# Kernel tuning notes

Hardware: AMD Instinct MI355X
Metric: run time of the kernel (lower is better)

## Reference

```python
import jax, jax.numpy as jnp
import numpy as np
import math

N, E = 50000, 800000
N_BASIS, N_ATOM, L = 32, 128, 2
START, STOP = 0.0, 10.0

_idx = [(i, j, L - i - j) for i in range(L + 1) for j in range(L + 1 - i)]
IP = np.array([t[0] for t in _idx], np.float32)
JP = np.array([t[1] for t in _idx], np.float32)
KP = np.array([t[2] for t in _idx], np.float32)
_d = np.array([math.factorial(a) * math.factorial(b) * math.factorial(c) for a, b, c in _idx], np.float32)
PREF2 = np.sqrt(math.factorial(L) / _d).astype(np.float32)  # [T], T = (L+1)(L+2)/2 = 6
OFFSETS = np.linspace(START, STOP, N_BASIS, dtype=np.float32)
WIDTH = np.float32(OFFSETS[1] - OFFSETS[0])


def _signed_pow(x, p):
    # matches torch.pow for negative base with integer-valued float exponent
    p = np.asarray(p)
    odd = (p.astype(np.int64) % 2 == 1)
    r = jnp.abs(x)[:, None] ** jnp.asarray(p)[None, :]
    return jnp.where((x < 0.0)[:, None] & jnp.asarray(odd)[None, :], -r, r)


def setup_inputs() -> dict:
    key = jax.random.key(0)
    ks = jax.random.split(key, 12)
    s = 0.05
    return {
        "feat": jax.random.normal(ks[0], (N, N_ATOM), jnp.float32),
        "dis_vec": jax.random.normal(ks[1], (E, 3), jnp.float32),
        "cj_w1": jax.random.normal(ks[2], (N_ATOM, N_ATOM), jnp.float32) * s,
        "cj_b1": jnp.zeros((N_ATOM,), jnp.float32),
        "cj_w2": jax.random.normal(ks[3], (N_ATOM, 1), jnp.float32) * s,
        "cj_b2": jnp.zeros((1,), jnp.float32),
        "msg_w1": jax.random.normal(ks[4], (N_BASIS, N_ATOM), jnp.float32) * s,
        "msg_b1": jnp.zeros((N_ATOM,), jnp.float32),
        "msg_w2": jax.random.normal(ks[5], (N_ATOM, N_ATOM), jnp.float32) * s,
        "msg_b2": jnp.zeros((N_ATOM,), jnp.float32),
        "filt_w1": jax.random.normal(ks[6], (IP.shape[0], IP.shape[0]), jnp.float32) * s,
        "filt_w2": jax.random.normal(ks[7], (IP.shape[0], 1), jnp.float32) * s,
        "filt_b2": jnp.zeros((1,), jnp.float32),
        "src": jax.random.randint(ks[8], (E,), 0, N, jnp.int32),
        "dst": jax.random.randint(ks[9], (E,), 0, N, jnp.int32),
    }


def reference(feat, dis_vec, cj_w1, cj_b1, cj_w2, cj_b2, msg_w1, msg_b1, msg_w2, msg_b2, filt_w1, filt_w2, filt_b2, src, dst):
    silu = jax.nn.silu  # swish
    # polynomial prefactor: [E, T]
    phix = _signed_pow(dis_vec[:, 0] + 1e-8, IP)
    phiy = _signed_pow(dis_vec[:, 1] + 1e-8, JP)
    phiz = _signed_pow(dis_vec[:, 2] + 1e-8, KP)
    prefactor = phix * phiy * phiz
    # gaussian basis: [E, n_basis] (cutoff_network is None -> C = 1)
    dis = jnp.linalg.norm(dis_vec + 1e-9, axis=-1)
    coeff = -0.5 / (WIDTH ** 2)
    g0 = jnp.exp(coeff * (dis[:, None] - jnp.asarray(OFFSETS)[None, :]) ** 2)
    # gauss: [E, n_basis, T]
    gauss = prefactor[:, None, :] * g0[:, :, None] * jnp.asarray(PREF2)[None, None, :]
    # cj = cj_mlp(feat): [N, 1]
    cj = silu(feat @ cj_w1 + cj_b1) @ cj_w2 + cj_b2
    # e_mul_v: gather dst-node scalar onto edges; copy_e_sum(g.reverse()): scatter-sum to src nodes
    fij = gauss * cj[dst][:, :, None]  # [E, n_basis, T]
    agg = jax.ops.segment_sum(fij, src, num_segments=N)  # [N, n_basis, T]
    f2 = jnp.sum(agg ** 2, axis=-1)  # [N, n_basis]
    msg_in = f2 / (jnp.linalg.norm(f2 + 1e-9, axis=-1, keepdims=True) + 1.0)
    msg_out = silu(msg_in @ msg_w1 + msg_b1) @ msg_w2 + msg_b2  # [N, n_atom_basis]
    gn = gauss / (jnp.linalg.norm(gauss + 1e-8, axis=-1) + 1.0)[..., None]
    filt = (silu(gn @ filt_w1) @ filt_w2 + filt_b2)[..., 0]  # [E, n_basis]
    return msg_out, filt
```

## Files before the change

kernel.cpp:

```cpp
#include <hip/hip_runtime.h>
#include <math.h>

#define N_NODES 50000
#define N_EDGES 800000
#define NB 32
#define NA 128

constexpr double STEP_D = 10.0 / 31.0;
constexpr float  STEP_F = (float)(10.0 / 31.0);
constexpr float  COEFF  = -0.5f / (STEP_F * STEP_F);
constexpr float  R2     = 1.41421356237309515f;
constexpr float  INV_STEP = 3.1f;
constexpr float  HWIN   = 2.05f;

__device__ __forceinline__ float fast_rcp(float x) {
    return __builtin_amdgcn_rcpf(x);
}

__device__ __forceinline__ float silu_f(float x) {
    return x * fast_rcp(1.0f + __expf(-x));
}

__global__ __launch_bounds__(256) void k_cj(const float* __restrict__ feat,
                                            const float* __restrict__ w1,
                                            const float* __restrict__ b1,
                                            const float* __restrict__ w2,
                                            const float* __restrict__ b2,
                                            float* __restrict__ cj) {
    __shared__ float fls[64 * 128];
    int tid = threadIdx.x;
    int jq  = tid & 31;
    int ng  = tid >> 5;
    int j0  = jq * 4;
    int n0  = blockIdx.x * 64;

    {
        const float4* fp = (const float4*)feat;
        int base = n0 * 32;
        int maxi = N_NODES * 32 - 1;
#pragma unroll
        for (int r = 0; r < 8; r++) {
            int idx = base + r * 256 + tid;
            ((float4*)fls)[r * 256 + tid] = fp[min(idx, maxi)];
        }
    }
    __syncthreads();

    float4 bv = *(const float4*)&b1[j0];
    float h[8][4];
#pragma unroll
    for (int i = 0; i < 8; i++) {
        h[i][0] = bv.x; h[i][1] = bv.y; h[i][2] = bv.z; h[i][3] = bv.w;
    }
    for (int kb = 0; kb < 128; kb += 4) {
        float4 wv[4];
#pragma unroll
        for (int u = 0; u < 4; u++) wv[u] = *(const float4*)&w1[(kb + u) * 128 + j0];
#pragma unroll
        for (int i = 0; i < 8; i++) {
            float4 f4 = *(const float4*)&fls[(ng * 8 + i) * 128 + kb];
            h[i][0] = fmaf(f4.x, wv[0].x, h[i][0]);
            h[i][1] = fmaf(f4.x, wv[0].y, h[i][1]);
            h[i][2] = fmaf(f4.x, wv[0].z, h[i][2]);
            h[i][3] = fmaf(f4.x, wv[0].w, h[i][3]);
            h[i][0] = fmaf(f4.y, wv[1].x, h[i][0]);
            h[i][1] = fmaf(f4.y, wv[1].y, h[i][1]);
            h[i][2] = fmaf(f4.y, wv[1].z, h[i][2]);
            h[i][3] = fmaf(f4.y, wv[1].w, h[i][3]);
            h[i][0] = fmaf(f4.z, wv[2].x, h[i][0]);
            h[i][1] = fmaf(f4.z, wv[2].y, h[i][1]);
            h[i][2] = fmaf(f4.z, wv[2].z, h[i][2]);
            h[i][3] = fmaf(f4.z, wv[2].w, h[i][3]);
            h[i][0] = fmaf(f4.w, wv[3].x, h[i][0]);
            h[i][1] = fmaf(f4.w, wv[3].y, h[i][1]);
            h[i][2] = fmaf(f4.w, wv[3].z, h[i][2]);
            h[i][3] = fmaf(f4.w, wv[3].w, h[i][3]);
        }
    }
    float4 w2v = *(const float4*)&w2[j0];
    float keep = 0.f;
#pragma unroll
    for (int i = 0; i < 8; i++) {
        float v = silu_f(h[i][0]) * w2v.x + silu_f(h[i][1]) * w2v.y
                + silu_f(h[i][2]) * w2v.z + silu_f(h[i][3]) * w2v.w;
#pragma unroll
        for (int m = 1; m < 32; m <<= 1) v += __shfl_xor(v, m, 64);
        if (jq == i) keep = v;
    }
    if (jq < 8) {
        int n = n0 + ng * 8 + jq;
        if (n < N_NODES) cj[n] = b2[0] + keep;
    }
}

__global__ void k_count(const int* __restrict__ src, int* __restrict__ cnt) {
    int e = blockIdx.x * 256 + threadIdx.x;
    if (e < N_EDGES) atomicAdd(&cnt[src[e]], 1);
}

__global__ void k_scan1(const int* __restrict__ cnt, int* __restrict__ offs,
                        int* __restrict__ bsum) {
    __shared__ int s[1024];
    int i = blockIdx.x * 1024 + threadIdx.x;
    int v = (i < N_NODES) ? cnt[i] : 0;
    s[threadIdx.x] = v;
    __syncthreads();
    for (int o = 1; o < 1024; o <<= 1) {
        int t = (threadIdx.x >= (unsigned)o) ? s[threadIdx.x - o] : 0;
        __syncthreads();
        s[threadIdx.x] += t;
        __syncthreads();
    }
    if (i < N_NODES) offs[i] = s[threadIdx.x] - v;
    if (threadIdx.x == 1023) bsum[blockIdx.x] = s[1023];
}

__global__ void k_scan2(const int* __restrict__ bsum, int* __restrict__ bbase, int nb) {
    if (threadIdx.x == 0) {
        int r = 0;
        for (int i = 0; i < nb; i++) { bbase[i] = r; r += bsum[i]; }
    }
}

__global__ void k_scan3(int* __restrict__ offs, const int* __restrict__ bbase,
                        int* __restrict__ cursor) {
    int i = blockIdx.x * 1024 + threadIdx.x;
    if (i < N_NODES) {
        int v = offs[i] + bbase[blockIdx.x];
        offs[i] = v;
        cursor[i] = v;
    }
}

__global__ void k_scatter(const int* __restrict__ src, const int* __restrict__ dst,
                          const float* __restrict__ dis_vec, const float* __restrict__ cj,
                          int* __restrict__ cursor, float* __restrict__ sedge) {
    int e = blockIdx.x * 256 + threadIdx.x;
    if (e >= N_EDGES) return;
    int p = atomicAdd(&cursor[src[e]], 1);
    float dx = dis_vec[3 * e], dy = dis_vec[3 * e + 1], dz = dis_vec[3 * e + 2];
    float cjd = cj[dst[e]];
    float ax = dx + 1e-9f, ay = dy + 1e-9f, az = dz + 1e-9f;
    float dis = sqrtf(ax * ax + ay * ay + az * az);
    float x = dx + 1e-8f, y = dy + 1e-8f, z = dz + 1e-8f;
    float4* op = (float4*)(sedge + (size_t)p * 8);
    op[0] = make_float4(dis, z * z * cjd, y * z * R2 * cjd, y * y * cjd);
    op[1] = make_float4(x * z * R2 * cjd, x * y * R2 * cjd, x * x * cjd, 0.f);
}

__global__ __launch_bounds__(256) void k_agg(const float* __restrict__ sedge,
                                             const int* __restrict__ offs,
                                             const int* __restrict__ cnt,
                                             float* __restrict__ msg_in) {
    int lane = threadIdx.x & 63;
    int n = blockIdx.x * 4 + (threadIdx.x >> 6);
    if (n >= N_NODES) return;
    int b = lane >> 1, th = lane & 1;
    float offb = (float)((double)b * STEP_D);
    int beg = offs[n];
    int deg = cnt[n];
    const float4* sp = (const float4*)sedge + (size_t)beg * 2;
    float a0 = 0.f, a1 = 0.f, a2 = 0.f;
    int i = 0;
    for (; i + 2 <= deg; i += 2) {
        float4 r0 = sp[0], r1 = sp[1], r2 = sp[2], r3 = sp[3];
        sp += 4;
        float dd0 = r0.x - offb;
        float dd1 = r2.x - offb;
        float g0 = __expf(COEFF * dd0 * dd0);
        float g1 = __expf(COEFF * dd1 * dd1);
        float w00 = th ? r1.x : r0.y, w01 = th ? r1.y : r0.z, w02 = th ? r1.z : r0.w;
        float w10 = th ? r3.x : r2.y, w11 = th ? r3.y : r2.z, w12 = th ? r3.z : r2.w;
        a0 = fmaf(g0, w00, a0);
        a1 = fmaf(g0, w01, a1);
        a2 = fmaf(g0, w02, a2);
        a0 = fmaf(g1, w10, a0);
        a1 = fmaf(g1, w11, a1);
        a2 = fmaf(g1, w12, a2);
    }
    if (i < deg) {
        float4 r0 = sp[0], r1 = sp[1];
        float dd0 = r0.x - offb;
        float g0 = __expf(COEFF * dd0 * dd0);
        float w00 = th ? r1.x : r0.y, w01 = th ? r1.y : r0.z, w02 = th ? r1.z : r0.w;
        a0 = fmaf(g0, w00, a0);
        a1 = fmaf(g0, w01, a1);
        a2 = fmaf(g0, w02, a2);
    }
    float s = a0 * a0 + a1 * a1 + a2 * a2;
    float f2 = s + __shfl_xor(s, 1, 64);
    float p = f2 + 1e-9f;
    p = p * p;
    float tot = p;
#pragma unroll
    for (int m = 1; m < 64; m <<= 1) tot += __shfl_xor(tot, m, 64);
    float nrm = sqrtf(0.5f * tot);
    float val = f2 * fast_rcp(nrm + 1.0f);
    if (th == 0) msg_in[(size_t)n * NB + b] = val;
}

__global__ __launch_bounds__(256) void k_msg(const float* __restrict__ msg_in,
                                             const float* __restrict__ w1,
                                             const float* __restrict__ b1,
                                             const float* __restrict__ w2,
                                             const float* __restrict__ b2,
                                             float* __restrict__ out) {
    __shared__ float mi[64 * 32];
    __shared__ float sh[64 * 128];
    int tid = threadIdx.x;
    int jq  = tid & 31;
    int ng  = tid >> 5;
    int j0  = jq * 4;
    int n0  = blockIdx.x * 64;

    {
        const float4* srcp = (const float4*)msg_in;
        int base = n0 * 8;
        int maxi = N_NODES * 8 - 1;
#pragma unroll
        for (int r = 0; r < 2; r++) {
            int idx = base + r * 256 + tid;
            ((float4*)mi)[r * 256 + tid] = srcp[min(idx, maxi)];
        }
    }
    __syncthreads();

    float4 b1v = *(const float4*)&b1[j0];
    float h[8][4];
#pragma unroll
    for (int i = 0; i < 8; i++) {
        h[i][0] = b1v.x; h[i][1] = b1v.y; h[i][2] = b1v.z; h[i][3] = b1v.w;
    }
#pragma unroll
    for (int bb = 0; bb < 32; bb += 4) {
        float4 wv[4];
#pragma unroll
        for (int u = 0; u < 4; u++) wv[u] = *(const float4*)&w1[(bb + u) * 128 + j0];
#pragma unroll
        for (int i = 0; i < 8; i++) {
            float4 m4 = *(const float4*)&mi[(ng * 8 + i) * 32 + bb];
            h[i][0] = fmaf(m4.x, wv[0].x, h[i][0]);
            h[i][1] = fmaf(m4.x, wv[0].y, h[i][1]);
            h[i][2] = fmaf(m4.x, wv[0].z, h[i][2]);
            h[i][3] = fmaf(m4.x, wv[0].w, h[i][3]);
            h[i][0] = fmaf(m4.y, wv[1].x, h[i][0]);
            h[i][1] = fmaf(m4.y, wv[1].y, h[i][1]);
            h[i][2] = fmaf(m4.y, wv[1].z, h[i][2]);
            h[i][3] = fmaf(m4.y, wv[1].w, h[i][3]);
            h[i][0] = fmaf(m4.z, wv[2].x, h[i][0]);
            h[i][1] = fmaf(m4.z, wv[2].y, h[i][1]);
            h[i][2] = fmaf(m4.z, wv[2].z, h[i][2]);
            h[i][3] = fmaf(m4.z, wv[2].w, h[i][3]);
            h[i][0] = fmaf(m4.w, wv[3].x, h[i][0]);
            h[i][1] = fmaf(m4.w, wv[3].y, h[i][1]);
            h[i][2] = fmaf(m4.w, wv[3].z, h[i][2]);
            h[i][3] = fmaf(m4.w, wv[3].w, h[i][3]);
        }
    }
#pragma unroll
    for (int i = 0; i < 8; i++) {
        float4 sv = make_float4(silu_f(h[i][0]), silu_f(h[i][1]),
                                silu_f(h[i][2]), silu_f(h[i][3]));
        *(float4*)&sh[(ng * 8 + i) * 128 + j0] = sv;
    }
    __syncthreads();

    float4 b2v = *(const float4*)&b2[j0];
    float acc[8][4];
#pragma unroll
    for (int i = 0; i < 8; i++) {
        acc[i][0] = b2v.x; acc[i][1] = b2v.y; acc[i][2] = b2v.z; acc[i][3] = b2v.w;
    }
    for (int hb = 0; hb < 128; hb += 4) {
        float4 wv[4];
#pragma unroll
        for (int u = 0; u < 4; u++) wv[u] = *(const float4*)&w2[(hb + u) * 128 + j0];
#pragma unroll
        for (int i = 0; i < 8; i++) {
            float4 s4 = *(const float4*)&sh[(ng * 8 + i) * 128 + hb];
            acc[i][0] = fmaf(s4.x, wv[0].x, acc[i][0]);
            acc[i][1] = fmaf(s4.x, wv[0].y, acc[i][1]);
            acc[i][2] = fmaf(s4.x, wv[0].z, acc[i][2]);
            acc[i][3] = fmaf(s4.x, wv[0].w, acc[i][3]);
            acc[i][0] = fmaf(s4.y, wv[1].x, acc[i][0]);
            acc[i][1] = fmaf(s4.y, wv[1].y, acc[i][1]);
            acc[i][2] = fmaf(s4.y, wv[1].z, acc[i][2]);
            acc[i][3] = fmaf(s4.y, wv[1].w, acc[i][3]);
            acc[i][0] = fmaf(s4.z, wv[2].x, acc[i][0]);
            acc[i][1] = fmaf(s4.z, wv[2].y, acc[i][1]);
            acc[i][2] = fmaf(s4.z, wv[2].z, acc[i][2]);
            acc[i][3] = fmaf(s4.z, wv[2].w, acc[i][3]);
            acc[i][0] = fmaf(s4.w, wv[3].x, acc[i][0]);
            acc[i][1] = fmaf(s4.w, wv[3].y, acc[i][1]);
            acc[i][2] = fmaf(s4.w, wv[3].z, acc[i][2]);
            acc[i][3] = fmaf(s4.w, wv[3].w, acc[i][3]);
        }
    }
#pragma unroll
    for (int i = 0; i < 8; i++) {
        int n = n0 + ng * 8 + i;
        if (n < N_NODES) {
            *(float4*)&out[(size_t)n * 128 + j0] =
                make_float4(acc[i][0], acc[i][1], acc[i][2], acc[i][3]);
        }
    }
}

__global__ __launch_bounds__(256) void k_filt(const float* __restrict__ dis_vec,
                                              const float* __restrict__ fw1,
                                              const float* __restrict__ fw2,
                                              const float* __restrict__ fb2,
                                              float* __restrict__ out) {
    __shared__ float buf[256 * 36];
    int tid = threadIdx.x;
    int e = blockIdx.x * 256 + tid;
    if (e >= N_EDGES) return;
    float dx = dis_vec[3 * e], dy = dis_vec[3 * e + 1], dz = dis_vec[3 * e + 2];
    float ax = dx + 1e-9f, ay = dy + 1e-9f, az = dz + 1e-9f;
    float dis = sqrtf(ax * ax + ay * ay + az * az);
    float x = dx + 1e-8f, y = dy + 1e-8f, z = dz + 1e-8f;
    float pre[6];
    pre[0] = z * z;      pre[1] = y * z * R2; pre[2] = y * y;
    pre[3] = x * z * R2; pre[4] = x * y * R2; pre[5] = x * x;
    float A = 0.f, B = 0.f;
#pragma unroll
    for (int t = 0; t < 6; t++) { A = fmaf(pre[t], pre[t], A); B += pre[t]; }
    float q[6];
#pragma unroll
    for (int tp = 0; tp < 6; tp++) {
        float s = 0.f;
#pragma unroll
        for (int t = 0; t < 6; t++) s = fmaf(pre[t], fw1[t * 6 + tp], s);
        q[tp] = s;
    }
    float bias = fb2[0];
    float w2r[6];
#pragma unroll
    for (int t = 0; t < 6; t++) w2r[t] = fw2[t];

    float* row = &buf[tid * 36];
    float4 b4v = make_float4(bias, bias, bias, bias);
#pragma unroll
    for (int r = 0; r < 8; r++) ((float4*)row)[r] = b4v;

    int b_lo = (int)ceilf((dis - HWIN) * INV_STEP);
#pragma unroll
    for (int k = 0; k < 14; k++) {
        int b = b_lo + k;
        float offb = (float)((double)b * STEP_D);
        float dd = dis - offb;
        float g = __expf(COEFF * dd * dd);
        float ns = fmaf(g * g, A, fmaf(2e-8f * g, B, 6e-16f));
        float rn = fast_rcp(sqrtf(ns) + 1.0f);
        float s = g * rn;
        float o = bias;
#pragma unroll
        for (int tp = 0; tp < 6; tp++) o = fmaf(silu_f(s * q[tp]), w2r[tp], o);
        if ((unsigned)b < 32u) row[b] = o;
    }

    float4* orow = (float4*)(out + (size_t)e * 32);
#pragma unroll
    for (int r = 0; r < 8; r++) orow[r] = ((float4*)row)[r];
}

extern "C" void kernel_launch(void* const* d_in, const int* in_sizes, int n_in,
                              void* d_out, int out_size, void* d_ws, size_t ws_size,
                              hipStream_t stream) {
    (void)in_sizes; (void)n_in; (void)out_size; (void)ws_size;
    const float* feat    = (const float*)d_in[0];
    const float* dis_vec = (const float*)d_in[1];
    const float* cj_w1   = (const float*)d_in[2];
    const float* cj_b1   = (const float*)d_in[3];
    const float* cj_w2   = (const float*)d_in[4];
    const float* cj_b2   = (const float*)d_in[5];
    const float* msg_w1  = (const float*)d_in[6];
    const float* msg_b1  = (const float*)d_in[7];
    const float* msg_w2  = (const float*)d_in[8];
    const float* msg_b2  = (const float*)d_in[9];
    const float* filt_w1 = (const float*)d_in[10];
    const float* filt_w2 = (const float*)d_in[11];
    const float* filt_b2 = (const float*)d_in[12];
    const int*   src     = (const int*)d_in[13];
    const int*   dst     = (const int*)d_in[14];
    float* out = (float*)d_out;

    float* ws     = (float*)d_ws;
    float* cj     = ws;
    float* msg_in = cj + 50048;
    int*   cnt    = (int*)(msg_in + 1600256);
    int*   offs   = cnt + 50048;
    int*   cursor = offs + 50048;
    int*   bsum   = cursor + 50048;
    int*   bbase  = bsum + 64;
    float* sedge  = (float*)(bbase + 64);

    hipMemsetAsync(cnt, 0, N_NODES * sizeof(int), stream);

    k_cj<<<(N_NODES + 63) / 64, 256, 0, stream>>>(feat, cj_w1, cj_b1, cj_w2, cj_b2, cj);
    k_count<<<(N_EDGES + 255) / 256, 256, 0, stream>>>(src, cnt);
    k_scan1<<<49, 1024, 0, stream>>>(cnt, offs, bsum);
    k_scan2<<<1, 64, 0, stream>>>(bsum, bbase, 49);
    k_scan3<<<49, 1024, 0, stream>>>(offs, bbase, cursor);
    k_scatter<<<(N_EDGES + 255) / 256, 256, 0, stream>>>(src, dst, dis_vec, cj, cursor, sedge);
    k_agg<<<(N_NODES + 3) / 4, 256, 0, stream>>>(sedge, offs, cnt, msg_in);
    k_msg<<<(N_NODES + 63) / 64, 256, 0, stream>>>(msg_in, msg_w1, msg_b1, msg_w2, msg_b2, out);
    k_filt<<<(N_EDGES + 255) / 256, 256, 0, stream>>>(dis_vec, filt_w1, filt_w2, filt_b2,
                                                      out + (size_t)N_NODES * NA);
}
```

Baseline: 407.0 us.

## Fuse cj/count, single-block scan, and merge edge scatter with filter kernel

Merges the cj MLP and degree-count kernels into one launch that splits by block index. The three scan kernels become one single-block scan in which each thread serially handles 49 nodes. Edge scatter and filter computation are merged into one edge kernel, so dis_vec is read once and the prefactor work is shared. Filter output is now staged through shared memory and written with coalesced float4 stores. Together these reduce launch count and redundant global reads, but the single-block scan serialises work, and the fused edge kernel puts atomics and heavy math in the same kernel, which may raise register pressure.

```diff
diff --git a/kernel.cpp b/kernel.cpp
--- a/kernel.cpp
+++ b/kernel.cpp
@@ -5,6 +5,9 @@
 #define N_EDGES 800000
 #define NB 32
 #define NA 128
+#define CJ_BLOCKS 782
+#define CNT_BLOCKS 3125
+#define EDGE_BLOCKS 3125
 
 constexpr double STEP_D = 10.0 / 31.0;
 constexpr float  STEP_F = (float)(10.0 / 31.0);
@@ -21,18 +24,26 @@
     return x * fast_rcp(1.0f + __expf(-x));
 }
 
-__global__ __launch_bounds__(256) void k_cj(const float* __restrict__ feat,
-                                            const float* __restrict__ w1,
-                                            const float* __restrict__ b1,
-                                            const float* __restrict__ w2,
-                                            const float* __restrict__ b2,
-                                            float* __restrict__ cj) {
+__global__ __launch_bounds__(256) void k_cj_count(const float* __restrict__ feat,
+                                                  const float* __restrict__ w1,
+                                                  const float* __restrict__ b1,
+                                                  const float* __restrict__ w2,
+                                                  const float* __restrict__ b2,
+                                                  float* __restrict__ cj,
+                                                  const int* __restrict__ src,
+                                                  int* __restrict__ cnt) {
     __shared__ float fls[64 * 128];
     int tid = threadIdx.x;
+    int blk = blockIdx.x;
+    if (blk >= CJ_BLOCKS) {
+        int e = (blk - CJ_BLOCKS) * 256 + tid;
+        if (e < N_EDGES) atomicAdd(&cnt[src[e]], 1);
+        return;
+    }
     int jq  = tid & 31;
     int ng  = tid >> 5;
     int j0  = jq * 4;
-    int n0  = blockIdx.x * 64;
+    int n0  = blk * 64;
 
     {
         const float4* fp = (const float4*)feat;
@@ -93,59 +104,114 @@
     }
 }
 
-__global__ void k_count(const int* __restrict__ src, int* __restrict__ cnt) {
-    int e = blockIdx.x * 256 + threadIdx.x;
-    if (e < N_EDGES) atomicAdd(&cnt[src[e]], 1);
-}
-
-__global__ void k_scan1(const int* __restrict__ cnt, int* __restrict__ offs,
-                        int* __restrict__ bsum) {
+__global__ __launch_bounds__(1024) void k_scan(const int* __restrict__ cnt,
+                                               int* __restrict__ offs,
+                                               int* __restrict__ cursor) {
     __shared__ int s[1024];
-    int i = blockIdx.x * 1024 + threadIdx.x;
-    int v = (i < N_NODES) ? cnt[i] : 0;
-    s[threadIdx.x] = v;
+    int t = threadIdx.x;
+    int base = t * 49;
+    int lsum = 0;
+#pragma unroll 7
+    for (int i = 0; i < 49; i++) {
+        int idx = base + i;
+        lsum += (idx < N_NODES) ? cnt[idx] : 0;
+    }
+    s[t] = lsum;
     __syncthreads();
     for (int o = 1; o < 1024; o <<= 1) {
-        int t = (threadIdx.x >= (unsigned)o) ? s[threadIdx.x - o] : 0;
+        int v = (t >= o) ? s[t - o] : 0;
         __syncthreads();
-        s[threadIdx.x] += t;
+        s[t] += v;
         __syncthreads();
     }
-    if (i < N_NODES) offs[i] = s[threadIdx.x] - v;
-    if (threadIdx.x == 1023) bsum[blockIdx.x] = s[1023];
-}
-
-__global__ void k_scan2(const int* __restrict__ bsum, int* __restrict__ bbase, int nb) {
-    if (threadIdx.x == 0) {
-        int r = 0;
-        for (int i = 0; i < nb; i++) { bbase[i] = r; r += bsum[i]; }
-    }
-}
-
-__global__ void k_scan3(int* __restrict__ offs, const int* __restrict__ bbase,
-                        int* __restrict__ cursor) {
-    int i = blockIdx.x * 1024 + threadIdx.x;
-    if (i < N_NODES) {
-        int v = offs[i] + bbase[blockIdx.x];
-        offs[i] = v;
-        cursor[i] = v;
-    }
-}
-
-__global__ void k_scatter(const int* __restrict__ src, const int* __restrict__ dst,
-                          const float* __restrict__ dis_vec, const float* __restrict__ cj,
-                          int* __restrict__ cursor, float* __restrict__ sedge) {
-    int e = blockIdx.x * 256 + threadIdx.x;
-    if (e >= N_EDGES) return;
-    int p = atomicAdd(&cursor[src[e]], 1);
+    int run = (t > 0) ? s[t - 1] : 0;
+    for (int i = 0; i < 49; i++) {
+        int idx = base + i;
+        if (idx < N_NODES) {
+            offs[idx]   = run;
+            cursor[idx] = run;
+            run += cnt[idx];
+        }
+    }
+}
+
+__global__ __launch_bounds__(256) void k_edge(const int* __restrict__ src,
+                                              const int* __restrict__ dst,
+                                              const float* __restrict__ dis_vec,
+                                              const float* __restrict__ cj,
+                                              int* __restrict__ cursor,
+                                              float* __restrict__ sedge,
+                                              const float* __restrict__ fw1,
+                                              const float* __restrict__ fw2,
+                                              const float* __restrict__ fb2,
+                                              float* __restrict__ outf) {
+    __shared__ float buf[256 * 36];
+    int tid = threadIdx.x;
+    int e = blockIdx.x * 256 + tid;
+    int se = src[e];
+    int de = dst[e];
     float dx = dis_vec[3 * e], dy = dis_vec[3 * e + 1], dz = dis_vec[3 * e + 2];
-    float cjd = cj[dst[e]];
+    float cjd = cj[de];
+    int p = atomicAdd(&cursor[se], 1);
+
     float ax = dx + 1e-9f, ay = dy + 1e-9f, az = dz + 1e-9f;
     float dis = sqrtf(ax * ax + ay * ay + az * az);
     float x = dx + 1e-8f, y = dy + 1e-8f, z = dz + 1e-8f;
-    float4* op = (float4*)(sedge + (size_t)p * 8);
-    op[0] = make_float4(dis, z * z * cjd, y * z * R2 * cjd, y * y * cjd);
-    op[1] = make_float4(x * z * R2 * cjd, x * y * R2 * cjd, x * x * cjd, 0.f);
+    float pre[6];
+    pre[0] = z * z;      pre[1] = y * z * R2; pre[2] = y * y;
+    pre[3] = x * z * R2; pre[4] = x * y * R2; pre[5] = x * x;
+
+    {
+        float4* op = (float4*)(sedge + (size_t)p * 8);
+        op[0] = make_float4(dis, pre[0] * cjd, pre[1] * cjd, pre[2] * cjd);
+        op[1] = make_float4(pre[3] * cjd, pre[4] * cjd, pre[5] * cjd, 0.f);
+    }
+
+    float A = 0.f, B = 0.f;
+#pragma unroll
+    for (int t = 0; t < 6; t++) { A = fmaf(pre[t], pre[t], A); B += pre[t]; }
+    float q[6];
+#pragma unroll
+    for (int tp = 0; tp < 6; tp++) {
+        float s = 0.f;
+#pragma unroll
+        for (int t = 0; t < 6; t++) s = fmaf(pre[t], fw1[t * 6 + tp], s);
+        q[tp] = s;
+    }
+    float bias = fb2[0];
+    float w2r[6];
+#pragma unroll
+    for (int t = 0; t < 6; t++) w2r[t] = fw2[t];
+
+    float* row = &buf[tid * 36];
+    float4 b4v = make_float4(bias, bias, bias, bias);
+#pragma unroll
+    for (int r = 0; r < 8; r++) ((float4*)row)[r] = b4v;
+
+    int b_lo = (int)ceilf((dis - HWIN) * INV_STEP);
+#pragma unroll
+    for (int k = 0; k < 14; k++) {
+        int b = b_lo + k;
+        float offb = (float)((double)b * STEP_D);
+        float dd = dis - offb;
+        float g = __expf(COEFF * dd * dd);
+        float ns = fmaf(g * g, A, fmaf(2e-8f * g, B, 6e-16f));
+        float rn = fast_rcp(sqrtf(ns) + 1.0f);
+        float s = g * rn;
+        float o = bias;
+#pragma unroll
+        for (int tp = 0; tp < 6; tp++) o = fmaf(silu_f(s * q[tp]), w2r[tp], o);
+        if ((unsigned)b < 32u) row[b] = o;
+    }
+    __syncthreads();
+
+    float4* ob = (float4*)(outf + (size_t)blockIdx.x * (256 * 32));
+#pragma unroll
+    for (int r = 0; r < 8; r++) {
+        int g = r * 256 + tid;
+        int eloc = g >> 3, j = g & 7;
+        ob[g] = *(const float4*)&buf[eloc * 36 + j * 4];
+    }
 }
 
 __global__ __launch_bounds__(256) void k_agg(const float* __restrict__ sedge,
@@ -306,64 +372,6 @@
     }
 }
 
-__global__ __launch_bounds__(256) void k_filt(const float* __restrict__ dis_vec,
-                                              const float* __restrict__ fw1,
-                                              const float* __restrict__ fw2,
-                                              const float* __restrict__ fb2,
-                                              float* __restrict__ out) {
-    __shared__ float buf[256 * 36];
-    int tid = threadIdx.x;
-    int e = blockIdx.x * 256 + tid;
-    if (e >= N_EDGES) return;
-    float dx = dis_vec[3 * e], dy = dis_vec[3 * e + 1], dz = dis_vec[3 * e + 2];
-    float ax = dx + 1e-9f, ay = dy + 1e-9f, az = dz + 1e-9f;
-    float dis = sqrtf(ax * ax + ay * ay + az * az);
-    float x = dx + 1e-8f, y = dy + 1e-8f, z = dz + 1e-8f;
-    float pre[6];
-    pre[0] = z * z;      pre[1] = y * z * R2; pre[2] = y * y;
-    pre[3] = x * z * R2; pre[4] = x * y * R2; pre[5] = x * x;
-    float A = 0.f, B = 0.f;
-#pragma unroll
-    for (int t = 0; t < 6; t++) { A = fmaf(pre[t], pre[t], A); B += pre[t]; }
-    float q[6];
-#pragma unroll
-    for (int tp = 0; tp < 6; tp++) {
-        float s = 0.f;
-#pragma unroll
-        for (int t = 0; t < 6; t++) s = fmaf(pre[t], fw1[t * 6 + tp], s);
-        q[tp] = s;
-    }
-    float bias = fb2[0];
-    float w2r[6];
-#pragma unroll
-    for (int t = 0; t < 6; t++) w2r[t] = fw2[t];
-
-    float* row = &buf[tid * 36];
-    float4 b4v = make_float4(bias, bias, bias, bias);
-#pragma unroll
-    for (int r = 0; r < 8; r++) ((float4*)row)[r] = b4v;
-
-    int b_lo = (int)ceilf((dis - HWIN) * INV_STEP);
-#pragma unroll
-    for (int k = 0; k < 14; k++) {
-        int b = b_lo + k;
-        float offb = (float)((double)b * STEP_D);
-        float dd = dis - offb;
-        float g = __expf(COEFF * dd * dd);
-        float ns = fmaf(g * g, A, fmaf(2e-8f * g, B, 6e-16f));
-        float rn = fast_rcp(sqrtf(ns) + 1.0f);
-        float s = g * rn;
-        float o = bias;
-#pragma unroll
-        for (int tp = 0; tp < 6; tp++) o = fmaf(silu_f(s * q[tp]), w2r[tp], o);
-        if ((unsigned)b < 32u) row[b] = o;
-    }
-
-    float4* orow = (float4*)(out + (size_t)e * 32);
-#pragma unroll
-    for (int r = 0; r < 8; r++) orow[r] = ((float4*)row)[r];
-}
-
 extern "C" void kernel_launch(void* const* d_in, const int* in_sizes, int n_in,
                               void* d_out, int out_size, void* d_ws, size_t ws_size,
                               hipStream_t stream) {
@@ -397,14 +405,12 @@
 
     hipMemsetAsync(cnt, 0, N_NODES * sizeof(int), stream);
 
-    k_cj<<<(N_NODES + 63) / 64, 256, 0, stream>>>(feat, cj_w1, cj_b1, cj_w2, cj_b2, cj);
-    k_count<<<(N_EDGES + 255) / 256, 256, 0, stream>>>(src, cnt);
-    k_scan1<<<49, 1024, 0, stream>>>(cnt, offs, bsum);
-    k_scan2<<<1, 64, 0, stream>>>(bsum, bbase, 49);
-    k_scan3<<<49, 1024, 0, stream>>>(offs, bbase, cursor);
-    k_scatter<<<(N_EDGES + 255) / 256, 256, 0, stream>>>(src, dst, dis_vec, cj, cursor, sedge);
+    k_cj_count<<<CJ_BLOCKS + CNT_BLOCKS, 256, 0, stream>>>(feat, cj_w1, cj_b1, cj_w2,
+                                                           cj_b2, cj, src, cnt);
+    k_scan<<<1, 1024, 0, stream>>>(cnt, offs, cursor);
+    k_edge<<<EDGE_BLOCKS, 256, 0, stream>>>(src, dst, dis_vec, cj, cursor, sedge,
+                                            filt_w1, filt_w2, filt_b2,
+                                            out + (size_t)N_NODES * NA);
     k_agg<<<(N_NODES + 3) / 4, 256, 0, stream>>>(sedge, offs, cnt, msg_in);
     k_msg<<<(N_NODES + 63) / 64, 256, 0, stream>>>(msg_in, msg_w1, msg_b1, msg_w2, msg_b2, out);
-    k_filt<<<(N_EDGES + 255) / 256, 256, 0, stream>>>(dis_vec, filt_w1, filt_w2, filt_b2,
-                                                      out + (size_t)N_NODES * NA);
-}
+}
```

Measured after the change: 469.9 us. +15.5%, slower.
